# Optimization experiments

Hardware: AMD Instinct MI355X
Metric: run time of the kernel (lower is better)

## Reference

```python
import jax, jax.numpy as jnp
import numpy as np

N, E, IN_C, HID_C, OUT_C = 50000, 800000, 64, 64, 8
NEG_SLOPE = 0.2


def setup_inputs() -> dict:
    key = jax.random.key(0)
    ks = jax.random.split(key, 12)
    return {
        "x": jax.random.normal(ks[0], (N, IN_C), dtype=jnp.float32),
        "edge_index": jax.random.randint(ks[1], (2, E), 0, N, dtype=jnp.int64),
        "edge_value": jax.random.uniform(ks[2], (E,), dtype=jnp.float32),
        "W1": jax.random.normal(ks[3], (IN_C, HID_C), dtype=jnp.float32) * 0.1,
        "a1_src": jax.random.normal(ks[4], (HID_C,), dtype=jnp.float32) * 0.1,
        "a1_dst": jax.random.normal(ks[5], (HID_C,), dtype=jnp.float32) * 0.1,
        "b1": jnp.zeros((HID_C,), dtype=jnp.float32),
        "W2": jax.random.normal(ks[6], (HID_C, OUT_C), dtype=jnp.float32) * 0.1,
        "a2_src": jax.random.normal(ks[7], (OUT_C,), dtype=jnp.float32) * 0.1,
        "a2_dst": jax.random.normal(ks[8], (OUT_C,), dtype=jnp.float32) * 0.1,
        "b2": jnp.zeros((OUT_C,), dtype=jnp.float32),
    }


def _rgat_conv(x, src, dst, edge_value, W, a_src, a_dst, b, n_nodes):
    # Linear transform: [N, out_c]
    h = x @ W
    # Per-node attention halves, gathered per edge -> per-edge logit
    e_src = h @ a_src  # [N]
    e_dst = h @ a_dst  # [N]
    logits = jax.nn.leaky_relu(e_src[src] + e_dst[dst], negative_slope=NEG_SLOPE)  # [E]
    # Segment softmax over destination neighborhoods (numerically stable)
    m = jax.ops.segment_max(logits, dst, num_segments=n_nodes)  # [N]
    ex = jnp.exp(logits - m[dst])
    denom = jax.ops.segment_sum(ex, dst, num_segments=n_nodes)  # [N]
    alpha = ex / (denom[dst] + 1e-16)  # [E]
    # Edge-weighted messages, scatter-aggregate to destinations
    msg = (alpha * edge_value)[:, None] * h[src]  # [E, out_c]
    out = jax.ops.segment_sum(msg, dst, num_segments=n_nodes)  # [N, out_c]
    return out + b


def reference(x, edge_index, edge_value, W1, a1_src, a1_dst, b1, W2, a2_src, a2_dst, b2):
    src, dst = edge_index[0], edge_index[1]
    n = x.shape[0]
    hid = _rgat_conv(x, src, dst, edge_value, W1, a1_src, a1_dst, b1, n)
    hid = jax.nn.relu(hid)
    out = _rgat_conv(hid, src, dst, edge_value, W2, a2_src, a2_dst, b2, n)
    return jax.nn.log_softmax(out, axis=1)
```

## Files before the change

### kernel.cpp

```cpp
#include <hip/hip_runtime.h>
#include <hip/hip_fp16.h>
#include <math.h>


#define CHUNK 4096
#define NBKT  256
#define CAP   6144
#define NPW   4

typedef unsigned long long ull;
typedef float v2f __attribute__((ext_vector_type(2)));

struct PartSmem {
    int lhist[NBKT], lbase[NBKT], lcur[NBKT], gbase[NBKT];
    ull buf[CHUNK];
};
struct GemmSmem {
    float4 Wl[64 * 16];
    float  Xt[64 * 64];
};
union FusedSmem { PartSmem p; GemmSmem g; };


__global__ void __launch_bounds__(256) part_gemm_kernel(
    const int* __restrict__ src, const int* __restrict__ dst,
    const float* __restrict__ ev, int* __restrict__ bcnt,
    ull* __restrict__ ped, int E, int nchunks,
    const float* __restrict__ x, const float* __restrict__ W,
    const float* __restrict__ a_src, const float* __restrict__ a_dst,
    unsigned* __restrict__ h, float* __restrict__ es, float* __restrict__ ed,
    int N)
{
    __shared__ FusedSmem sm;
    const int t = threadIdx.x;

    if (blockIdx.x < nchunks) {
        int e0 = blockIdx.x * CHUNK;
        int cnt = min(CHUNK, E - e0);
        sm.p.lhist[t] = 0;
        __syncthreads();
        for (int i = t; i < cnt; i += 256)
            atomicAdd(&sm.p.lhist[dst[e0 + i] >> 8], 1);
        __syncthreads();
        int myc = sm.p.lhist[t];
        sm.p.lbase[t] = myc;
        __syncthreads();
        for (int o = 1; o < 256; o <<= 1) {
            int add = (t >= o) ? sm.p.lbase[t - o] : 0;
            __syncthreads();
            sm.p.lbase[t] += add;
            __syncthreads();
        }
        int excl = sm.p.lbase[t] - myc;
        sm.p.gbase[t] = myc ? atomicAdd(&bcnt[t], myc) : 0;
        __syncthreads();
        sm.p.lbase[t] = excl;
        sm.p.lcur[t] = excl;
        __syncthreads();
        for (int i = t; i < cnt; i += 256) {
            int e = e0 + i;
            int d = dst[e];
            int b = d >> 8;
            unsigned p = (unsigned)src[e] | ((unsigned)(d & 255) << 16)
                       | ((unsigned)b << 24);
            ull q = (ull)p | ((ull)__float_as_uint(ev[e]) << 32);
            int r = atomicAdd(&sm.p.lcur[b], 1);
            sm.p.buf[r] = q;
        }
        __syncthreads();
        for (int i = t; i < cnt; i += 256) {
            ull q = sm.p.buf[i];
            int b = (int)((q >> 24) & 255);
            ped[(size_t)b * CAP + sm.p.gbase[b] + i - sm.p.lbase[b]] = q;
        }
        return;
    }

    const int n0 = (blockIdx.x - nchunks) * 64;

    #pragma unroll
    for (int i = 0; i < 4; ++i)
        sm.g.Wl[t + i * 256] = ((const float4*)W)[t + i * 256];

    #pragma unroll
    for (int i = 0; i < 4; ++i) {
        int f   = t + i * 256;
        int row = f >> 4, kq = f & 15;
        int grow = n0 + row;
        float4 v = make_float4(0.f, 0.f, 0.f, 0.f);
        if (grow < N) v = ((const float4*)x)[(size_t)grow * 16 + kq];
        int rs = row ^ ((kq & 3) << 2);
        sm.g.Xt[(kq * 4 + 0) * 64 + rs] = v.x;
        sm.g.Xt[(kq * 4 + 1) * 64 + rs] = v.y;
        sm.g.Xt[(kq * 4 + 2) * 64 + rs] = v.z;
        sm.g.Xt[(kq * 4 + 3) * 64 + rs] = v.w;
    }

    const int tx = t & 15;
    const int ty = t >> 4;
    const float4 asv = ((const float4*)a_src)[tx];
    const float4 adv = ((const float4*)a_dst)[tx];
    __syncthreads();

    float4 acc0 = make_float4(0.f,0.f,0.f,0.f);
    float4 acc1 = make_float4(0.f,0.f,0.f,0.f);
    float4 acc2 = make_float4(0.f,0.f,0.f,0.f);
    float4 acc3 = make_float4(0.f,0.f,0.f,0.f);

    #pragma unroll 8
    for (int k = 0; k < 64; ++k) {
        int swz = (k >> 2) & 3;
        const float4 xr = *(const float4*)&sm.g.Xt[k * 64 + ((ty ^ swz) << 2)];
        const float4 wv = sm.g.Wl[k * 16 + tx];
        acc0.x += xr.x * wv.x; acc0.y += xr.x * wv.y;
        acc0.z += xr.x * wv.z; acc0.w += xr.x * wv.w;
        acc1.x += xr.y * wv.x; acc1.y += xr.y * wv.y;
        acc1.z += xr.y * wv.z; acc1.w += xr.y * wv.w;
        acc2.x += xr.z * wv.x; acc2.y += xr.z * wv.y;
        acc2.z += xr.z * wv.z; acc2.w += xr.z * wv.w;
        acc3.x += xr.w * wv.x; acc3.y += xr.w * wv.y;
        acc3.z += xr.w * wv.z; acc3.w += xr.w * wv.w;
    }

    float4 accs[4] = {acc0, acc1, acc2, acc3};
    #pragma unroll
    for (int r = 0; r < 4; ++r) {
        int grow = n0 + ty * 4 + r;
        float4 a = accs[r];
        if (grow < N) {
            int lo = __builtin_amdgcn_cvt_pk_fp8_f32(a.x, a.y, 0, false);
            int pk = __builtin_amdgcn_cvt_pk_fp8_f32(a.z, a.w, lo, true);
            h[(size_t)grow * 16 + tx] = (unsigned)pk;
        }
        float ps = a.x * asv.x + a.y * asv.y + a.z * asv.z + a.w * asv.w;
        float pd = a.x * adv.x + a.y * adv.y + a.z * adv.z + a.w * adv.w;
        #pragma unroll
        for (int o = 8; o > 0; o >>= 1) {
            ps += __shfl_xor(ps, o);
            pd += __shfl_xor(pd, o);
        }
        if (tx == 0 && grow < N) { es[grow] = ps; ed[grow] = pd; }
    }
}


__global__ void __launch_bounds__(1024) csr2_kernel(
    const ull* __restrict__ ped, const int* __restrict__ bcnt,
    int* __restrict__ off, int* __restrict__ deg,
    ull* __restrict__ csre, int N)
{
    __shared__ int cl[256], sc[256], cur[256];
    int b = blockIdx.x, t = threadIdx.x;
    const int cnt = min(bcnt[b], CAP);
    const size_t base = (size_t)b * CAP;
    if (t < 256) cl[t] = 0;
    __syncthreads();
    for (int i = t; i < cnt; i += 1024)
        atomicAdd(&cl[(int)((ped[base + i] >> 16) & 255)], 1);
    __syncthreads();
    int myc = (t < 256) ? cl[t] : 0;
    if (t < 256) sc[t] = myc;
    __syncthreads();
    for (int o = 1; o < 256; o <<= 1) {
        int add = (t >= o && t < 256) ? sc[t - o] : 0;
        __syncthreads();
        if (t < 256) sc[t] += add;
        __syncthreads();
    }
    if (t < 256) {
        int excl = sc[t] - myc;
        int node = b * 256 + t;
        if (node < N) { off[node] = (int)base + excl; deg[node] = myc; }
        cur[t] = excl;
    }
    __syncthreads();
    for (int i = t; i < cnt; i += 1024) {
        ull q = ped[base + i];
        int dloc = (int)((q >> 16) & 255);
        int pos = (int)base + atomicAdd(&cur[dloc], 1);
        csre[pos] = (q & 0xFFFFFFFF00000000ull) | (q & 0xFFFFull);
    }
}


#define UNPACK_ACC16(u, we)                                              \
    do {                                                                 \
        v2f f0a = __builtin_amdgcn_cvt_pk_f32_fp8((int)(u).x, false);    \
        v2f f0b = __builtin_amdgcn_cvt_pk_f32_fp8((int)(u).x, true);     \
        v2f f1a = __builtin_amdgcn_cvt_pk_f32_fp8((int)(u).y, false);    \
        v2f f1b = __builtin_amdgcn_cvt_pk_f32_fp8((int)(u).y, true);     \
        v2f f2a = __builtin_amdgcn_cvt_pk_f32_fp8((int)(u).z, false);    \
        v2f f2b = __builtin_amdgcn_cvt_pk_f32_fp8((int)(u).z, true);     \
        v2f f3a = __builtin_amdgcn_cvt_pk_f32_fp8((int)(u).w, false);    \
        v2f f3b = __builtin_amdgcn_cvt_pk_f32_fp8((int)(u).w, true);     \
        acc[0]  += (we) * f0a.x;  acc[1]  += (we) * f0a.y;               \
        acc[2]  += (we) * f0b.x;  acc[3]  += (we) * f0b.y;               \
        acc[4]  += (we) * f1a.x;  acc[5]  += (we) * f1a.y;               \
        acc[6]  += (we) * f1b.x;  acc[7]  += (we) * f1b.y;               \
        acc[8]  += (we) * f2a.x;  acc[9]  += (we) * f2a.y;               \
        acc[10] += (we) * f2b.x;  acc[11] += (we) * f2b.y;               \
        acc[12] += (we) * f3a.x;  acc[13] += (we) * f3a.y;               \
        acc[14] += (we) * f3b.x;  acc[15] += (we) * f3b.y;               \
    } while (0)

__global__ void __launch_bounds__(256) agg64_fused_kernel(
    const int* __restrict__ off, const int* __restrict__ deg,
    const ull* __restrict__ csre,
    const float* __restrict__ es, const float* __restrict__ ed,
    const unsigned* __restrict__ h, const float* __restrict__ b1,
    const float* __restrict__ W2, const float* __restrict__ a2s,
    const float* __restrict__ a2d, float* __restrict__ h2,
    float* __restrict__ es2, float* __restrict__ ed2, int N)
{
    const int wid = threadIdx.x >> 6, lane = threadIdx.x & 63;
    const int eslot = lane >> 2;
    const int q     = lane & 3;
    const int n0 = (blockIdx.x * 4 + wid) * NPW;
    if (n0 >= N) return;
    const int n1 = min(n0 + NPW, N);

    const int ch = 16 * q + 8 * ((lane >> 2) & 1) + 4 * ((lane >> 3) & 1)
                 + 2 * ((lane >> 4) & 1) + ((lane >> 5) & 1);
    const float b1c = b1[ch];
    float w2row[8];
    {
        const float4 wa = ((const float4*)(W2 + ch * 8))[0];
        const float4 wb = ((const float4*)(W2 + ch * 8))[1];
        w2row[0] = wa.x; w2row[1] = wa.y; w2row[2] = wa.z; w2row[3] = wa.w;
        w2row[4] = wb.x; w2row[5] = wb.y; w2row[6] = wb.z; w2row[7] = wb.w;
    }
    const int olane = 4 * (lane & 1) + 2 * ((lane >> 1) & 1) + ((lane >> 2) & 1);
    const float a2sv = a2s[olane], a2dv = a2d[olane];

    int offv = 0, degv = 0;
    float edv = 0.f;
    {
        int nn = n0 + (lane & (NPW - 1));
        if (nn < N) { offv = off[nn]; degv = deg[nn]; edv = ed[nn]; }
    }

    int svS; float evS, esS;
    uint4 puS;
    {
        int begX = __shfl(offv, 0);
        int cntX = min(__shfl(degv, 0), 64);
        int idxX = begX + min(lane, max(cntX, 1) - 1);
        ull recX = csre[idxX];
        svS = (int)(recX & 0xFFFFull);
        evS = __uint_as_float((unsigned)(recX >> 32));
        esS = es[svS];
        int s0 = __shfl(svS, eslot);
        puS = *(const uint4*)&h[(size_t)s0 * 16 + q * 4];
    }

    for (int n = n0; n < n1; ++n) {
        const int nl = n - n0;
        const int beg = __shfl(offv, nl);
        const int dg  = __shfl(degv, nl);
        const float edn = __shfl(edv, nl);
        const int cnt0 = min(dg, 64);

        const int sv = svS;
        float z = esS + edn;
        float l = z > 0.f ? z : 0.2f * z;
        float qv = (lane < cnt0) ? __expf(l) : 0.f;
        float den = qv;
        const float wv = qv * evS;

        const uint4 cu = puS;

        if (n + 1 < n1) {
            int begX = __shfl(offv, nl + 1);
            int cntX = min(__shfl(degv, nl + 1), 64);
            int idxX = begX + min(lane, max(cntX, 1) - 1);
            ull recX = csre[idxX];
            svS = (int)(recX & 0xFFFFull);
            evS = __uint_as_float((unsigned)(recX >> 32));
            esS = es[svS];
            int s0 = __shfl(svS, eslot);
            puS = *(const uint4*)&h[(size_t)s0 * 16 + q * 4];
        }

        float acc[16];
        #pragma unroll
        for (int k = 0; k < 16; ++k) acc[k] = 0.f;

        {
            float we = __shfl(wv, eslot);
            UNPACK_ACC16(cu, we);
        }
        for (int j = 16; j < cnt0; j += 16) {
            int   se = __shfl(sv, j + eslot);
            float we = __shfl(wv, j + eslot);
            const uint4 u = *(const uint4*)&h[(size_t)se * 16 + q * 4];
            UNPACK_ACC16(u, we);
        }
        for (int base2 = beg + 64; base2 < beg + dg; base2 += 64) {
            const int cnt = min(beg + dg - base2, 64);
            const int idx = base2 + min(lane, cnt - 1);
            const ull rec = csre[idx];
            const int sv2 = (int)(rec & 0xFFFFull);
            const float ev2 = __uint_as_float((unsigned)(rec >> 32));
            float z2 = es[sv2] + edn;
            float l2 = z2 > 0.f ? z2 : 0.2f * z2;
            float q2 = (lane < cnt) ? __expf(l2) : 0.f;
            den += q2;
            const float wv2 = q2 * ev2;
            for (int j = 0; j < cnt; j += 16) {
                int   se = __shfl(sv2, j + eslot);
                float we = __shfl(wv2, j + eslot);
                const uint4 u = *(const uint4*)&h[(size_t)se * 16 + q * 4];
                UNPACK_ACC16(u, we);
            }
        }

        float r8[8];
        {
            const bool hi = (lane & 4);
            #pragma unroll
            for (int k = 0; k < 8; ++k) {
                float keep = hi ? acc[k + 8] : acc[k];
                float send = hi ? acc[k]     : acc[k + 8];
                r8[k] = keep + __shfl_xor(send, 4);
            }
            den += __shfl_xor(den, 4);
        }
        float r4[4];
        {
            const bool hi = (lane & 8);
            #pragma unroll
            for (int k = 0; k < 4; ++k) {
                float keep = hi ? r8[k + 4] : r8[k];
                float send = hi ? r8[k]     : r8[k + 4];
                r4[k] = keep + __shfl_xor(send, 8);
            }
            den += __shfl_xor(den, 8);
        }
        float r2[2];
        {
            const bool hi = (lane & 16);
            #pragma unroll
            for (int k = 0; k < 2; ++k) {
                float keep = hi ? r4[k + 2] : r4[k];
                float send = hi ? r4[k]     : r4[k + 2];
                r2[k] = keep + __shfl_xor(send, 16);
            }
            den += __shfl_xor(den, 16);
        }
        float r1;
        {
            const bool hi = (lane & 32);
            float keep = hi ? r2[1] : r2[0];
            float send = hi ? r2[0] : r2[1];
            r1 = keep + __shfl_xor(send, 32);
            den += __shfl_xor(den, 32);
        }
        den += __shfl_xor(den, 1);
        den += __shfl_xor(den, 2);

        const float inv = 1.f / (den + 1e-16f);
        const float hid = fmaxf(r1 * inv + b1c, 0.f);

        float p[8];
        #pragma unroll
        for (int k = 0; k < 8; ++k) p[k] = hid * w2row[k];
        float s4[4];
        {
            const bool hi = (lane & 1);
            #pragma unroll
            for (int k = 0; k < 4; ++k) {
                float keep = hi ? p[k + 4] : p[k];
                float send = hi ? p[k]     : p[k + 4];
                s4[k] = keep + __shfl_xor(send, 1);
            }
        }
        float s2[2];
        {
            const bool hi = (lane & 2);
            #pragma unroll
            for (int k = 0; k < 2; ++k) {
                float keep = hi ? s4[k + 2] : s4[k];
                float send = hi ? s4[k]     : s4[k + 2];
                s2[k] = keep + __shfl_xor(send, 2);
            }
        }
        float s1;
        {
            const bool hi = (lane & 4);
            float keep = hi ? s2[1] : s2[0];
            float send = hi ? s2[0] : s2[1];
            s1 = keep + __shfl_xor(send, 4);
        }
        s1 += __shfl_xor(s1, 8);
        s1 += __shfl_xor(s1, 16);
        s1 += __shfl_xor(s1, 32);

        float ts = s1 * a2sv, td = s1 * a2dv;
        ts += __shfl_xor(ts, 1); td += __shfl_xor(td, 1);
        ts += __shfl_xor(ts, 2); td += __shfl_xor(td, 2);
        ts += __shfl_xor(ts, 4); td += __shfl_xor(td, 4);

        if (lane < 8) h2[(size_t)n * 8 + olane] = s1;
        if (lane == 0) { es2[n] = ts; ed2[n] = td; }
    }
}


__global__ void __launch_bounds__(256) agg8_lsm_kernel(
    const int* __restrict__ off, const int* __restrict__ deg,
    const ull* __restrict__ csre,
    const float* __restrict__ es, const float* __restrict__ ed,
    const float* __restrict__ h2, const float* __restrict__ b,
    float* __restrict__ out, int N)
{
    const int wid = threadIdx.x >> 6, lane = threadIdx.x & 63;
    const int eslot = lane >> 1;
    const int hh = lane & 1;
    const int n0 = (blockIdx.x * 4 + wid) * NPW;
    if (n0 >= N) return;
    const int n1 = min(n0 + NPW, N);

    const int ch = 4 * (lane & 1) + 2 * ((lane >> 1) & 1) + ((lane >> 2) & 1);
    const float bc = b[ch];

    int offv = 0, degv = 0;
    float edv = 0.f;
    {
        int nn = n0 + (lane & (NPW - 1));
        if (nn < N) { offv = off[nn]; degv = deg[nn]; edv = ed[nn]; }
    }

    int svS; float evS, esS;
    float4 pf;
    {
        int begX = __shfl(offv, 0);
        int cntX = min(__shfl(degv, 0), 64);
        int idxX = begX + min(lane, max(cntX, 1) - 1);
        ull recX = csre[idxX];
        svS = (int)(recX & 0xFFFFull);
        evS = __uint_as_float((unsigned)(recX >> 32));
        esS = es[svS];
        int s0 = __shfl(svS, eslot);
        pf = *(const float4*)&h2[(size_t)s0 * 8 + 4 * hh];
    }

    for (int n = n0; n < n1; ++n) {
        const int nl = n - n0;
        const int beg = __shfl(offv, nl);
        const int dg  = __shfl(degv, nl);
        const float edn = __shfl(edv, nl);
        const int cnt0 = min(dg, 64);

        const int sv = svS;
        float z = esS + edn;
        float l = z > 0.f ? z : 0.2f * z;
        float qv = (lane < cnt0) ? __expf(l) : 0.f;
        float den = qv;
        const float wv = qv * evS;

        const float4 cf = pf;

        if (n + 1 < n1) {
            int begX = __shfl(offv, nl + 1);
            int cntX = min(__shfl(degv, nl + 1), 64);
            int idxX = begX + min(lane, max(cntX, 1) - 1);
            ull recX = csre[idxX];
            svS = (int)(recX & 0xFFFFull);
            evS = __uint_as_float((unsigned)(recX >> 32));
            esS = es[svS];
            int s0 = __shfl(svS, eslot);
            pf = *(const float4*)&h2[(size_t)s0 * 8 + 4 * hh];
        }

        float acc[4];
        {
            float we = __shfl(wv, eslot);
            acc[0] = we * cf.x; acc[1] = we * cf.y;
            acc[2] = we * cf.z; acc[3] = we * cf.w;
        }
        for (int j = 32; j < cnt0; j += 32) {
            int   se = __shfl(sv, j + eslot);
            float we = __shfl(wv, j + eslot);
            const float4 f = *(const float4*)&h2[(size_t)se * 8 + 4 * hh];
            acc[0] += we * f.x; acc[1] += we * f.y;
            acc[2] += we * f.z; acc[3] += we * f.w;
        }
        for (int base2 = beg + 64; base2 < beg + dg; base2 += 64) {
            const int cnt = min(beg + dg - base2, 64);
            const int idx = base2 + min(lane, cnt - 1);
            const ull rec = csre[idx];
            const int sv2 = (int)(rec & 0xFFFFull);
            const float ev2 = __uint_as_float((unsigned)(rec >> 32));
            float z2 = es[sv2] + edn;
            float l2 = z2 > 0.f ? z2 : 0.2f * z2;
            float q2 = (lane < cnt) ? __expf(l2) : 0.f;
            den += q2;
            const float wv2 = q2 * ev2;
            for (int j = 0; j < cnt; j += 32) {
                int   se = __shfl(sv2, j + eslot);
                float we = __shfl(wv2, j + eslot);
                const float4 f = *(const float4*)&h2[(size_t)se * 8 + 4 * hh];
                acc[0] += we * f.x; acc[1] += we * f.y;
                acc[2] += we * f.z; acc[3] += we * f.w;
            }
        }

        float r2[2];
        {
            const bool hi = (lane & 2);
            #pragma unroll
            for (int k = 0; k < 2; ++k) {
                float keep = hi ? acc[k + 2] : acc[k];
                float send = hi ? acc[k]     : acc[k + 2];
                r2[k] = keep + __shfl_xor(send, 2);
            }
            den += __shfl_xor(den, 2);
        }
        float r1;
        {
            const bool hi = (lane & 4);
            float keep = hi ? r2[1] : r2[0];
            float send = hi ? r2[0] : r2[1];
            r1 = keep + __shfl_xor(send, 4);
            den += __shfl_xor(den, 4);
        }
        r1 += __shfl_xor(r1, 8);   den += __shfl_xor(den, 8);
        r1 += __shfl_xor(r1, 16);  den += __shfl_xor(den, 16);
        r1 += __shfl_xor(r1, 32);  den += __shfl_xor(den, 32);
        den += __shfl_xor(den, 1);

        const float inv = 1.f / (den + 1e-16f);
        const float v = r1 * inv + bc;

        float vm = v;
        vm = fmaxf(vm, __shfl_xor(vm, 1));
        vm = fmaxf(vm, __shfl_xor(vm, 2));
        vm = fmaxf(vm, __shfl_xor(vm, 4));
        float s = __expf(v - vm);
        s += __shfl_xor(s, 1);
        s += __shfl_xor(s, 2);
        s += __shfl_xor(s, 4);
        float lse = vm + logf(s);
        if (lane < 8)
            out[(size_t)n * 8 + ch] = v - lse;
    }
}


extern "C" void kernel_launch(void* const* d_in, const int* in_sizes, int n_in,
                              void* d_out, int out_size, void* d_ws, size_t ws_size,
                              hipStream_t stream)
{
    const float* x   = (const float*)d_in[0];
    const int*   ei  = (const int*)d_in[1];
    const float* ev  = (const float*)d_in[2];
    const float* W1  = (const float*)d_in[3];
    const float* a1s = (const float*)d_in[4];
    const float* a1d = (const float*)d_in[5];
    const float* b1  = (const float*)d_in[6];
    const float* W2  = (const float*)d_in[7];
    const float* a2s = (const float*)d_in[8];
    const float* a2d = (const float*)d_in[9];
    const float* b2  = (const float*)d_in[10];
    float* out = (float*)d_out;

    const int N = in_sizes[0] / 64;
    const int E = in_sizes[2];
    const int* srcp = ei;
    const int* dstp = ei + E;
    const int nchunks = (E + CHUNK - 1) / CHUNK;
    const int ngemm   = (N + 63) / 64;
    const int nbuck = (N + 255) / 256;
    const int nodes_per_block = 4 * NPW;

    ull*   ped  = (ull*)d_ws;
    ull*   csre = ped + (size_t)NBKT * CAP;
    int*   bcnt = (int*)(csre + (size_t)NBKT * CAP);
    int*   off  = bcnt + NBKT;
    int*   deg  = off + N;
    float* es1  = (float*)(deg + N);
    float* ed1  = es1 + N;
    float* es2  = ed1 + N;
    float* ed2  = es2 + N;
    unsigned* h1 = (unsigned*)(ed2 + N);
    float* h2   = (float*)(h1 + (size_t)N * 16);

    hipMemsetAsync(bcnt, 0, NBKT * sizeof(int), stream);

    part_gemm_kernel<<<nchunks + ngemm, 256, 0, stream>>>(
        srcp, dstp, ev, bcnt, ped, E, nchunks,
        x, W1, a1s, a1d, h1, es1, ed1, N);

    csr2_kernel<<<nbuck, 1024, 0, stream>>>(ped, bcnt, off, deg, csre, N);

    agg64_fused_kernel<<<(N + nodes_per_block - 1) / nodes_per_block, 256, 0, stream>>>(
        off, deg, csre, es1, ed1, h1, b1, W2, a2s, a2d, h2, es2, ed2, N);

    agg8_lsm_kernel<<<(N + nodes_per_block - 1) / nodes_per_block, 256, 0, stream>>>(
        off, deg, csre, es2, ed2, h2, b2, out, N);
}
```

Before: 156.6 us.

## Map sub-wave lane groups to individual nodes in both aggregation kernels

Both aggregation kernels are restructured so that each wave handles several destination nodes at once. In the 64-channel kernel an 8-lane group owns one node, and in the 8-channel kernel a 4-lane group owns one node, instead of a whole wave looping over four nodes with 64-edge batches. The aim is to recover the lanes left idle on low-degree nodes (average degree is about 16), to shorten the cross-lane reductions, and to remove the software prefetch logic. In exchange, each lane issues narrower gathers, W2 is staged through shared memory, and divergence appears when nodes in the same wave have very different degrees.

```diff
diff --git a/kernel.cpp b/kernel.cpp
--- a/kernel.cpp
+++ b/kernel.cpp
@@ -6,7 +6,6 @@
 #define CHUNK 4096
 #define NBKT  256
 #define CAP   6144
-#define NPW   4
 
 typedef unsigned long long ull;
 typedef float v2f __attribute__((ext_vector_type(2)));
@@ -183,26 +182,6 @@
 }
 
 
-#define UNPACK_ACC16(u, we)                                              \
-    do {                                                                 \
-        v2f f0a = __builtin_amdgcn_cvt_pk_f32_fp8((int)(u).x, false);    \
-        v2f f0b = __builtin_amdgcn_cvt_pk_f32_fp8((int)(u).x, true);     \
-        v2f f1a = __builtin_amdgcn_cvt_pk_f32_fp8((int)(u).y, false);    \
-        v2f f1b = __builtin_amdgcn_cvt_pk_f32_fp8((int)(u).y, true);     \
-        v2f f2a = __builtin_amdgcn_cvt_pk_f32_fp8((int)(u).z, false);    \
-        v2f f2b = __builtin_amdgcn_cvt_pk_f32_fp8((int)(u).z, true);     \
-        v2f f3a = __builtin_amdgcn_cvt_pk_f32_fp8((int)(u).w, false);    \
-        v2f f3b = __builtin_amdgcn_cvt_pk_f32_fp8((int)(u).w, true);     \
-        acc[0]  += (we) * f0a.x;  acc[1]  += (we) * f0a.y;               \
-        acc[2]  += (we) * f0b.x;  acc[3]  += (we) * f0b.y;               \
-        acc[4]  += (we) * f1a.x;  acc[5]  += (we) * f1a.y;               \
-        acc[6]  += (we) * f1b.x;  acc[7]  += (we) * f1b.y;               \
-        acc[8]  += (we) * f2a.x;  acc[9]  += (we) * f2a.y;               \
-        acc[10] += (we) * f2b.x;  acc[11] += (we) * f2b.y;               \
-        acc[12] += (we) * f3a.x;  acc[13] += (we) * f3a.y;               \
-        acc[14] += (we) * f3b.x;  acc[15] += (we) * f3b.y;               \
-    } while (0)
-
 __global__ void __launch_bounds__(256) agg64_fused_kernel(
     const int* __restrict__ off, const int* __restrict__ deg,
     const ull* __restrict__ csre,
@@ -212,197 +191,121 @@
     const float* __restrict__ a2d, float* __restrict__ h2,
     float* __restrict__ es2, float* __restrict__ ed2, int N)
 {
-    const int wid = threadIdx.x >> 6, lane = threadIdx.x & 63;
-    const int eslot = lane >> 2;
-    const int q     = lane & 3;
-    const int n0 = (blockIdx.x * 4 + wid) * NPW;
-    if (n0 >= N) return;
-    const int n1 = min(n0 + NPW, N);
-
-    const int ch = 16 * q + 8 * ((lane >> 2) & 1) + 4 * ((lane >> 3) & 1)
-                 + 2 * ((lane >> 4) & 1) + ((lane >> 5) & 1);
-    const float b1c = b1[ch];
-    float w2row[8];
+    __shared__ float W2s[64 * 8];
+    const int t = threadIdx.x;
+    if (t < 128) ((float4*)W2s)[t] = ((const float4*)W2)[t];
+
+    const int wid = t >> 6, lane = t & 63;
+    const int grp = lane >> 3;
+    const int sl  = lane & 7;
+    const int gbase = grp << 3;
+    const int n = (blockIdx.x * 4 + wid) * 8 + grp;
+    __syncthreads();
+    if (n >= N) return;
+
+    const int   beg = off[n];
+    const int   dg  = deg[n];
+    const float edn = ed[n];
+
+    const float4 b1a = *(const float4*)&b1[sl * 8];
+    const float4 b1b = *(const float4*)&b1[sl * 8 + 4];
+
+    float acc[8];
+    #pragma unroll
+    for (int k = 0; k < 8; ++k) acc[k] = 0.f;
+    float den = 0.f;
+
+    for (int j0 = 0; j0 < dg; j0 += 8) {
+        const int jj  = j0 + sl;
+        const int idx = beg + min(jj, dg - 1);
+        const ull rec = csre[idx];
+        const int sv  = (int)(rec & 0xFFFFull);
+        const float evv = __uint_as_float((unsigned)(rec >> 32));
+        float z = es[sv] + edn;
+        float l = z > 0.f ? z : 0.2f * z;
+        float q = (jj < dg) ? __expf(l) : 0.f;
+        den += q;
+        const float w = q * evv;
+        #pragma unroll
+        for (int ts = 0; ts < 8; ++ts) {
+            const int   svt = __shfl(sv, gbase + ts);
+            const float wt  = __shfl(w,  gbase + ts);
+            const uint2 u = *(const uint2*)&h[(size_t)svt * 16 + sl * 2];
+            v2f fa = __builtin_amdgcn_cvt_pk_f32_fp8((int)u.x, false);
+            v2f fb = __builtin_amdgcn_cvt_pk_f32_fp8((int)u.x, true);
+            v2f fc = __builtin_amdgcn_cvt_pk_f32_fp8((int)u.y, false);
+            v2f fd = __builtin_amdgcn_cvt_pk_f32_fp8((int)u.y, true);
+            acc[0] += wt * fa.x; acc[1] += wt * fa.y;
+            acc[2] += wt * fb.x; acc[3] += wt * fb.y;
+            acc[4] += wt * fc.x; acc[5] += wt * fc.y;
+            acc[6] += wt * fd.x; acc[7] += wt * fd.y;
+        }
+    }
+
+    den += __shfl_xor(den, 1);
+    den += __shfl_xor(den, 2);
+    den += __shfl_xor(den, 4);
+    const float inv = 1.f / (den + 1e-16f);
+
+    float hid[8];
+    hid[0] = fmaxf(acc[0] * inv + b1a.x, 0.f);
+    hid[1] = fmaxf(acc[1] * inv + b1a.y, 0.f);
+    hid[2] = fmaxf(acc[2] * inv + b1a.z, 0.f);
+    hid[3] = fmaxf(acc[3] * inv + b1a.w, 0.f);
+    hid[4] = fmaxf(acc[4] * inv + b1b.x, 0.f);
+    hid[5] = fmaxf(acc[5] * inv + b1b.y, 0.f);
+    hid[6] = fmaxf(acc[6] * inv + b1b.z, 0.f);
+    hid[7] = fmaxf(acc[7] * inv + b1b.w, 0.f);
+
+    float p[8];
+    #pragma unroll
+    for (int o = 0; o < 8; ++o) p[o] = 0.f;
+    #pragma unroll
+    for (int k = 0; k < 8; ++k) {
+        const float4 wA = *(const float4*)&W2s[(sl * 8 + k) * 8];
+        const float4 wB = *(const float4*)&W2s[(sl * 8 + k) * 8 + 4];
+        p[0] += hid[k] * wA.x; p[1] += hid[k] * wA.y;
+        p[2] += hid[k] * wA.z; p[3] += hid[k] * wA.w;
+        p[4] += hid[k] * wB.x; p[5] += hid[k] * wB.y;
+        p[6] += hid[k] * wB.z; p[7] += hid[k] * wB.w;
+    }
+    float s4[4];
     {
-        const float4 wa = ((const float4*)(W2 + ch * 8))[0];
-        const float4 wb = ((const float4*)(W2 + ch * 8))[1];
-        w2row[0] = wa.x; w2row[1] = wa.y; w2row[2] = wa.z; w2row[3] = wa.w;
-        w2row[4] = wb.x; w2row[5] = wb.y; w2row[6] = wb.z; w2row[7] = wb.w;
-    }
-    const int olane = 4 * (lane & 1) + 2 * ((lane >> 1) & 1) + ((lane >> 2) & 1);
-    const float a2sv = a2s[olane], a2dv = a2d[olane];
-
-    int offv = 0, degv = 0;
-    float edv = 0.f;
+        const bool hi = (sl & 1);
+        #pragma unroll
+        for (int k = 0; k < 4; ++k) {
+            float keep = hi ? p[k + 4] : p[k];
+            float send = hi ? p[k]     : p[k + 4];
+            s4[k] = keep + __shfl_xor(send, 1);
+        }
+    }
+    float s2[2];
     {
-        int nn = n0 + (lane & (NPW - 1));
-        if (nn < N) { offv = off[nn]; degv = deg[nn]; edv = ed[nn]; }
-    }
-
-    int svS; float evS, esS;
-    uint4 puS;
+        const bool hi = (sl & 2);
+        #pragma unroll
+        for (int k = 0; k < 2; ++k) {
+            float keep = hi ? s4[k + 2] : s4[k];
+            float send = hi ? s4[k]     : s4[k + 2];
+            s2[k] = keep + __shfl_xor(send, 2);
+        }
+    }
+    float s1;
     {
-        int begX = __shfl(offv, 0);
-        int cntX = min(__shfl(degv, 0), 64);
-        int idxX = begX + min(lane, max(cntX, 1) - 1);
-        ull recX = csre[idxX];
-        svS = (int)(recX & 0xFFFFull);
-        evS = __uint_as_float((unsigned)(recX >> 32));
-        esS = es[svS];
-        int s0 = __shfl(svS, eslot);
-        puS = *(const uint4*)&h[(size_t)s0 * 16 + q * 4];
-    }
-
-    for (int n = n0; n < n1; ++n) {
-        const int nl = n - n0;
-        const int beg = __shfl(offv, nl);
-        const int dg  = __shfl(degv, nl);
-        const float edn = __shfl(edv, nl);
-        const int cnt0 = min(dg, 64);
-
-        const int sv = svS;
-        float z = esS + edn;
-        float l = z > 0.f ? z : 0.2f * z;
-        float qv = (lane < cnt0) ? __expf(l) : 0.f;
-        float den = qv;
-        const float wv = qv * evS;
-
-        const uint4 cu = puS;
-
-        if (n + 1 < n1) {
-            int begX = __shfl(offv, nl + 1);
-            int cntX = min(__shfl(degv, nl + 1), 64);
-            int idxX = begX + min(lane, max(cntX, 1) - 1);
-            ull recX = csre[idxX];
-            svS = (int)(recX & 0xFFFFull);
-            evS = __uint_as_float((unsigned)(recX >> 32));
-            esS = es[svS];
-            int s0 = __shfl(svS, eslot);
-            puS = *(const uint4*)&h[(size_t)s0 * 16 + q * 4];
-        }
-
-        float acc[16];
-        #pragma unroll
-        for (int k = 0; k < 16; ++k) acc[k] = 0.f;
-
-        {
-            float we = __shfl(wv, eslot);
-            UNPACK_ACC16(cu, we);
-        }
-        for (int j = 16; j < cnt0; j += 16) {
-            int   se = __shfl(sv, j + eslot);
-            float we = __shfl(wv, j + eslot);
-            const uint4 u = *(const uint4*)&h[(size_t)se * 16 + q * 4];
-            UNPACK_ACC16(u, we);
-        }
-        for (int base2 = beg + 64; base2 < beg + dg; base2 += 64) {
-            const int cnt = min(beg + dg - base2, 64);
-            const int idx = base2 + min(lane, cnt - 1);
-            const ull rec = csre[idx];
-            const int sv2 = (int)(rec & 0xFFFFull);
-            const float ev2 = __uint_as_float((unsigned)(rec >> 32));
-            float z2 = es[sv2] + edn;
-            float l2 = z2 > 0.f ? z2 : 0.2f * z2;
-            float q2 = (lane < cnt) ? __expf(l2) : 0.f;
-            den += q2;
-            const float wv2 = q2 * ev2;
-            for (int j = 0; j < cnt; j += 16) {
-                int   se = __shfl(sv2, j + eslot);
-                float we = __shfl(wv2, j + eslot);
-                const uint4 u = *(const uint4*)&h[(size_t)se * 16 + q * 4];
-                UNPACK_ACC16(u, we);
-            }
-        }
-
-        float r8[8];
-        {
-            const bool hi = (lane & 4);
-            #pragma unroll
-            for (int k = 0; k < 8; ++k) {
-                float keep = hi ? acc[k + 8] : acc[k];
-                float send = hi ? acc[k]     : acc[k + 8];
-                r8[k] = keep + __shfl_xor(send, 4);
-            }
-            den += __shfl_xor(den, 4);
-        }
-        float r4[4];
-        {
-            const bool hi = (lane & 8);
-            #pragma unroll
-            for (int k = 0; k < 4; ++k) {
-                float keep = hi ? r8[k + 4] : r8[k];
-                float send = hi ? r8[k]     : r8[k + 4];
-                r4[k] = keep + __shfl_xor(send, 8);
-            }
-            den += __shfl_xor(den, 8);
-        }
-        float r2[2];
-        {
-            const bool hi = (lane & 16);
-            #pragma unroll
-            for (int k = 0; k < 2; ++k) {
-                float keep = hi ? r4[k + 2] : r4[k];
-                float send = hi ? r4[k]     : r4[k + 2];
-                r2[k] = keep + __shfl_xor(send, 16);
-            }
-            den += __shfl_xor(den, 16);
-        }
-        float r1;
-        {
-            const bool hi = (lane & 32);
-            float keep = hi ? r2[1] : r2[0];
-            float send = hi ? r2[0] : r2[1];
-            r1 = keep + __shfl_xor(send, 32);
-            den += __shfl_xor(den, 32);
-        }
-        den += __shfl_xor(den, 1);
-        den += __shfl_xor(den, 2);
-
-        const float inv = 1.f / (den + 1e-16f);
-        const float hid = fmaxf(r1 * inv + b1c, 0.f);
-
-        float p[8];
-        #pragma unroll
-        for (int k = 0; k < 8; ++k) p[k] = hid * w2row[k];
-        float s4[4];
-        {
-            const bool hi = (lane & 1);
-            #pragma unroll
-            for (int k = 0; k < 4; ++k) {
-                float keep = hi ? p[k + 4] : p[k];
-                float send = hi ? p[k]     : p[k + 4];
-                s4[k] = keep + __shfl_xor(send, 1);
-            }
-        }
-        float s2[2];
-        {
-            const bool hi = (lane & 2);
-            #pragma unroll
-            for (int k = 0; k < 2; ++k) {
-                float keep = hi ? s4[k + 2] : s4[k];
-                float send = hi ? s4[k]     : s4[k + 2];
-                s2[k] = keep + __shfl_xor(send, 2);
-            }
-        }
-        float s1;
-        {
-            const bool hi = (lane & 4);
-            float keep = hi ? s2[1] : s2[0];
-            float send = hi ? s2[0] : s2[1];
-            s1 = keep + __shfl_xor(send, 4);
-        }
-        s1 += __shfl_xor(s1, 8);
-        s1 += __shfl_xor(s1, 16);
-        s1 += __shfl_xor(s1, 32);
-
-        float ts = s1 * a2sv, td = s1 * a2dv;
-        ts += __shfl_xor(ts, 1); td += __shfl_xor(td, 1);
-        ts += __shfl_xor(ts, 2); td += __shfl_xor(td, 2);
-        ts += __shfl_xor(ts, 4); td += __shfl_xor(td, 4);
-
-        if (lane < 8) h2[(size_t)n * 8 + olane] = s1;
-        if (lane == 0) { es2[n] = ts; ed2[n] = td; }
-    }
+        const bool hi = (sl & 4);
+        float keep = hi ? s2[1] : s2[0];
+        float send = hi ? s2[0] : s2[1];
+        s1 = keep + __shfl_xor(send, 4);
+    }
+    const int olane = 4 * (sl & 1) + 2 * ((sl >> 1) & 1) + ((sl >> 2) & 1);
+
+    float ts = s1 * a2s[olane];
+    float td = s1 * a2d[olane];
+    ts += __shfl_xor(ts, 1); td += __shfl_xor(td, 1);
+    ts += __shfl_xor(ts, 2); td += __shfl_xor(td, 2);
+    ts += __shfl_xor(ts, 4); td += __shfl_xor(td, 4);
+
+    h2[(size_t)n * 8 + olane] = s1;
+    if (sl == 0) { es2[n] = ts; ed2[n] = td; }
 }
 
 
@@ -413,137 +316,56 @@
     const float* __restrict__ h2, const float* __restrict__ b,
     float* __restrict__ out, int N)
 {
-    const int wid = threadIdx.x >> 6, lane = threadIdx.x & 63;
-    const int eslot = lane >> 1;
-    const int hh = lane & 1;
-    const int n0 = (blockIdx.x * 4 + wid) * NPW;
-    if (n0 >= N) return;
-    const int n1 = min(n0 + NPW, N);
-
-    const int ch = 4 * (lane & 1) + 2 * ((lane >> 1) & 1) + ((lane >> 2) & 1);
-    const float bc = b[ch];
-
-    int offv = 0, degv = 0;
-    float edv = 0.f;
-    {
-        int nn = n0 + (lane & (NPW - 1));
-        if (nn < N) { offv = off[nn]; degv = deg[nn]; edv = ed[nn]; }
-    }
-
-    int svS; float evS, esS;
-    float4 pf;
-    {
-        int begX = __shfl(offv, 0);
-        int cntX = min(__shfl(degv, 0), 64);
-        int idxX = begX + min(lane, max(cntX, 1) - 1);
-        ull recX = csre[idxX];
-        svS = (int)(recX & 0xFFFFull);
-        evS = __uint_as_float((unsigned)(recX >> 32));
-        esS = es[svS];
-        int s0 = __shfl(svS, eslot);
-        pf = *(const float4*)&h2[(size_t)s0 * 8 + 4 * hh];
-    }
-
-    for (int n = n0; n < n1; ++n) {
-        const int nl = n - n0;
-        const int beg = __shfl(offv, nl);
-        const int dg  = __shfl(degv, nl);
-        const float edn = __shfl(edv, nl);
-        const int cnt0 = min(dg, 64);
-
-        const int sv = svS;
-        float z = esS + edn;
+    const int t = threadIdx.x;
+    const int wid = t >> 6, lane = t & 63;
+    const int grp = lane >> 2;
+    const int sl  = lane & 3;
+    const int gbase = grp << 2;
+    const int n = (blockIdx.x * 4 + wid) * 16 + grp;
+    if (n >= N) return;
+
+    const int   beg = off[n];
+    const int   dg  = deg[n];
+    const float edn = ed[n];
+    const float bc0 = b[2 * sl], bc1 = b[2 * sl + 1];
+
+    float a0 = 0.f, a1 = 0.f, den = 0.f;
+
+    for (int j0 = 0; j0 < dg; j0 += 4) {
+        const int jj  = j0 + sl;
+        const int idx = beg + min(jj, dg - 1);
+        const ull rec = csre[idx];
+        const int sv  = (int)(rec & 0xFFFFull);
+        const float evv = __uint_as_float((unsigned)(rec >> 32));
+        float z = es[sv] + edn;
         float l = z > 0.f ? z : 0.2f * z;
-        float qv = (lane < cnt0) ? __expf(l) : 0.f;
-        float den = qv;
-        const float wv = qv * evS;
-
-        const float4 cf = pf;
-
-        if (n + 1 < n1) {
-            int begX = __shfl(offv, nl + 1);
-            int cntX = min(__shfl(degv, nl + 1), 64);
-            int idxX = begX + min(lane, max(cntX, 1) - 1);
-            ull recX = csre[idxX];
-            svS = (int)(recX & 0xFFFFull);
-            evS = __uint_as_float((unsigned)(recX >> 32));
-            esS = es[svS];
-            int s0 = __shfl(svS, eslot);
-            pf = *(const float4*)&h2[(size_t)s0 * 8 + 4 * hh];
-        }
-
-        float acc[4];
-        {
-            float we = __shfl(wv, eslot);
-            acc[0] = we * cf.x; acc[1] = we * cf.y;
-            acc[2] = we * cf.z; acc[3] = we * cf.w;
-        }
-        for (int j = 32; j < cnt0; j += 32) {
-            int   se = __shfl(sv, j + eslot);
-            float we = __shfl(wv, j + eslot);
-            const float4 f = *(const float4*)&h2[(size_t)se * 8 + 4 * hh];
-            acc[0] += we * f.x; acc[1] += we * f.y;
-            acc[2] += we * f.z; acc[3] += we * f.w;
-        }
-        for (int base2 = beg + 64; base2 < beg + dg; base2 += 64) {
-            const int cnt = min(beg + dg - base2, 64);
-            const int idx = base2 + min(lane, cnt - 1);
-            const ull rec = csre[idx];
-            const int sv2 = (int)(rec & 0xFFFFull);
-            const float ev2 = __uint_as_float((unsigned)(rec >> 32));
-            float z2 = es[sv2] + edn;
-            float l2 = z2 > 0.f ? z2 : 0.2f * z2;
-            float q2 = (lane < cnt) ? __expf(l2) : 0.f;
-            den += q2;
-            const float wv2 = q2 * ev2;
-            for (int j = 0; j < cnt; j += 32) {
-                int   se = __shfl(sv2, j + eslot);
-                float we = __shfl(wv2, j + eslot);
-                const float4 f = *(const float4*)&h2[(size_t)se * 8 + 4 * hh];
-                acc[0] += we * f.x; acc[1] += we * f.y;
-                acc[2] += we * f.z; acc[3] += we * f.w;
-            }
-        }
-
-        float r2[2];
-        {
-            const bool hi = (lane & 2);
-            #pragma unroll
-            for (int k = 0; k < 2; ++k) {
-                float keep = hi ? acc[k + 2] : acc[k];
-                float send = hi ? acc[k]     : acc[k + 2];
-                r2[k] = keep + __shfl_xor(send, 2);
-            }
-            den += __shfl_xor(den, 2);
-        }
-        float r1;
-        {
-            const bool hi = (lane & 4);
-            float keep = hi ? r2[1] : r2[0];
-            float send = hi ? r2[0] : r2[1];
-            r1 = keep + __shfl_xor(send, 4);
-            den += __shfl_xor(den, 4);
-        }
-        r1 += __shfl_xor(r1, 8);   den += __shfl_xor(den, 8);
-        r1 += __shfl_xor(r1, 16);  den += __shfl_xor(den, 16);
-        r1 += __shfl_xor(r1, 32);  den += __shfl_xor(den, 32);
-        den += __shfl_xor(den, 1);
-
-        const float inv = 1.f / (den + 1e-16f);
-        const float v = r1 * inv + bc;
-
-        float vm = v;
-        vm = fmaxf(vm, __shfl_xor(vm, 1));
-        vm = fmaxf(vm, __shfl_xor(vm, 2));
-        vm = fmaxf(vm, __shfl_xor(vm, 4));
-        float s = __expf(v - vm);
-        s += __shfl_xor(s, 1);
-        s += __shfl_xor(s, 2);
-        s += __shfl_xor(s, 4);
-        float lse = vm + logf(s);
-        if (lane < 8)
-            out[(size_t)n * 8 + ch] = v - lse;
-    }
+        float q = (jj < dg) ? __expf(l) : 0.f;
+        den += q;
+        const float w = q * evv;
+        #pragma unroll
+        for (int ts = 0; ts < 4; ++ts) {
+            const int   svt = __shfl(sv, gbase + ts);
+            const float wt  = __shfl(w,  gbase + ts);
+            const float2 f = *(const float2*)&h2[(size_t)svt * 8 + 2 * sl];
+            a0 += wt * f.x;
+            a1 += wt * f.y;
+        }
+    }
+
+    den += __shfl_xor(den, 1);
+    den += __shfl_xor(den, 2);
+    const float inv = 1.f / (den + 1e-16f);
+    float v0 = a0 * inv + bc0;
+    float v1 = a1 * inv + bc1;
+
+    float vm = fmaxf(v0, v1);
+    vm = fmaxf(vm, __shfl_xor(vm, 1));
+    vm = fmaxf(vm, __shfl_xor(vm, 2));
+    float s = __expf(v0 - vm) + __expf(v1 - vm);
+    s += __shfl_xor(s, 1);
+    s += __shfl_xor(s, 2);
+    float lse = vm + logf(s);
+    *(float2*)&out[(size_t)n * 8 + 2 * sl] = make_float2(v0 - lse, v1 - lse);
 }
 
 
@@ -571,7 +393,6 @@
     const int nchunks = (E + CHUNK - 1) / CHUNK;
     const int ngemm   = (N + 63) / 64;
     const int nbuck = (N + 255) / 256;
-    const int nodes_per_block = 4 * NPW;
 
     ull*   ped  = (ull*)d_ws;
     ull*   csre = ped + (size_t)NBKT * CAP;
@@ -593,9 +414,9 @@
 
     csr2_kernel<<<nbuck, 1024, 0, stream>>>(ped, bcnt, off, deg, csre, N);
 
-    agg64_fused_kernel<<<(N + nodes_per_block - 1) / nodes_per_block, 256, 0, stream>>>(
+    agg64_fused_kernel<<<(N + 31) / 32, 256, 0, stream>>>(
         off, deg, csre, es1, ed1, h1, b1, W2, a2s, a2d, h2, es2, ed2, N);
 
-    agg8_lsm_kernel<<<(N + nodes_per_block - 1) / nodes_per_block, 256, 0, stream>>>(
+    agg8_lsm_kernel<<<(N + 63) / 64, 256, 0, stream>>>(
         off, deg, csre, es2, ed2, h2, b2, out, N);
 }
```

Measured after the change: 144.1 us. -8.0%, faster.
